# Kernel tuning notes

Hardware: AMD Instinct MI355X
Metric: run time of the kernel (lower is better)

## Reference

```python
import jax, jax.numpy as jnp
import numpy as np

B, S, DIM, H = 2, 2048, 1024, 16
HD = DIM // H  # head dim = 64


def setup_inputs() -> dict:
    key = jax.random.key(0)
    ks = jax.random.split(key, 10)
    scale = 1.0 / np.sqrt(DIM)
    x = jax.random.normal(ks[0], (B, S, DIM), dtype=jnp.float32)
    # per-head projection weights stacked over heads: [H, DIM, HD]
    Wq = jax.random.normal(ks[1], (H, DIM, HD), dtype=jnp.float32) * scale
    bq = jax.random.normal(ks[2], (H, HD), dtype=jnp.float32) * 0.01
    Wk = jax.random.normal(ks[3], (H, DIM, HD), dtype=jnp.float32) * scale
    bk = jax.random.normal(ks[4], (H, HD), dtype=jnp.float32) * 0.01
    Wv = jax.random.normal(ks[5], (H, DIM, HD), dtype=jnp.float32) * scale
    bv = jax.random.normal(ks[6], (H, HD), dtype=jnp.float32) * 0.01
    # output linear: [DIM, DIM]
    Wo = jax.random.normal(ks[7], (DIM, DIM), dtype=jnp.float32) * scale
    bo = jax.random.normal(ks[8], (DIM,), dtype=jnp.float32) * 0.01
    return {"x": x, "Wq": Wq, "bq": bq, "Wk": Wk, "bk": bk,
            "Wv": Wv, "bv": bv, "Wo": Wo, "bo": bo}


def reference(x, Wq, bq, Wk, bk, Wv, bv, Wo, bo):
    # per-head projections: [B, H, S, HD]
    q = jnp.einsum('bsd,hde->bhse', x, Wq) + bq[None, :, None, :]
    k = jnp.einsum('bsd,hde->bhse', x, Wk) + bk[None, :, None, :]
    v = jnp.einsum('bsd,hde->bhse', x, Wv) + bv[None, :, None, :]
    # causal attention scores: [B, H, S, S], scaled by sqrt(head_dim)
    scores = jnp.einsum('bhse,bhte->bhst', q, k) / jnp.sqrt(jnp.float32(HD))
    causal = jnp.tril(jnp.ones((S, S), dtype=bool))
    scores = jnp.where(causal[None, None], scores, -jnp.inf)
    attn = jax.nn.softmax(scores, axis=-1)
    out = jnp.einsum('bhst,bhte->bhse', attn, v)  # [B, H, S, HD]
    # concat heads in order -> [B, S, DIM]
    out = out.transpose(0, 2, 1, 3).reshape(B, S, DIM)
    return out @ Wo + bo
```

## Files before the change

### kernel.cpp

```cpp
#include <hip/hip_runtime.h>

typedef _Float16 half8 __attribute__((ext_vector_type(8)));
typedef _Float16 half4 __attribute__((ext_vector_type(4)));
typedef float f32x4 __attribute__((ext_vector_type(4)));

#define MFMA32(a, b, c) __builtin_amdgcn_mfma_f32_16x16x32_f16((a), (b), (c), 0, 0, 0)
#define MFMA16(a, b, c) __builtin_amdgcn_mfma_f32_16x16x16f16((a), (b), (c), 0, 0, 0)

static constexpr int Bc = 2, Sc = 2048, DIMc = 1024, Hc = 16, HDc = 64;
static constexpr int Mc = Bc * Sc;
static constexpr int NQKV = 3 * DIMc;

__device__ __forceinline__ void gl_lds16(const _Float16* g, _Float16* l) {
  __builtin_amdgcn_global_load_lds(
      (const __attribute__((address_space(1))) void*)g,
      (__attribute__((address_space(3))) void*)l, 16, 0, 0);
}


__global__ __launch_bounds__(256) void k_prep_all(
    const float* __restrict__ x, const float* __restrict__ Wq,
    const float* __restrict__ Wk, const float* __restrict__ Wv,
    const float* __restrict__ Wo, _Float16* __restrict__ xh,
    _Float16* __restrict__ WallT, _Float16* __restrict__ WoT) {
  __shared__ float Ls[64 * 65];
  const int bx = blockIdx.x, tid = threadIdx.x;
  if (bx < 2048) {
    const int i = bx * 256 + tid;
    const float4* xf = (const float4*)x;
    float4 a = xf[i * 2], b = xf[i * 2 + 1];
    half8 hv;
    hv[0] = (_Float16)a.x; hv[1] = (_Float16)a.y;
    hv[2] = (_Float16)a.z; hv[3] = (_Float16)a.w;
    hv[4] = (_Float16)b.x; hv[5] = (_Float16)b.y;
    hv[6] = (_Float16)b.z; hv[7] = (_Float16)b.w;
    *(half8*)&xh[(size_t)i * 8] = hv;
    return;
  }
  int b2 = bx - 2048;
  if (b2 < 768) {
    const int dt = b2 & 15, ph = b2 >> 4;
    const int p = ph >> 4, h = ph & 15;
    const float* W = (p == 0) ? Wq : (p == 1) ? Wk : Wv;
    for (int c = tid; c < 4096; c += 256) {
      int dr = c >> 6, e = c & 63;
      Ls[e * 65 + dr] = W[h * 65536 + (dt * 64 + dr) * 64 + e];
    }
    __syncthreads();
    for (int c = tid; c < 4096; c += 256) {
      int e = c >> 6, dr = c & 63;
      WallT[(size_t)(p * 1024 + h * 64 + e) * 1024 + dt * 64 + dr] = (_Float16)Ls[e * 65 + dr];
    }
  } else {
    int b3 = b2 - 768;
    const int dt = b3 & 15, nt = b3 >> 4;
    for (int c = tid; c < 4096; c += 256) {
      int dr = c >> 6, nl = c & 63;
      Ls[nl * 65 + dr] = Wo[(dt * 64 + dr) * 1024 + nt * 64 + nl];
    }
    __syncthreads();
    for (int c = tid; c < 4096; c += 256) {
      int nl = c >> 6, dr = c & 63;
      WoT[(size_t)(nt * 64 + nl) * 1024 + dt * 64 + dr] = (_Float16)Ls[nl * 65 + dr];
    }
  }
}


#define STAGE_AB(buf, kk0)                                                     \
    for (int it = 0; it < 2; ++it) {                                           \
      int idx = it * 256 + tid;                                                \
      int row = idx >> 2, scb = (idx & 3) ^ ((row >> 1) & 3);                  \
      gl_lds16(&A[(size_t)(m0 + row) * DIMc + (kk0) + scb * 8],                \
               &As[buf][(it * 256 + wave * 64) * 8]);                          \
    }                                                                          \
    for (int it = 0; it < 2; ++it) {                                           \
      int idx = it * 256 + tid;                                                \
      int row = idx >> 2, scb = (idx & 3) ^ ((row >> 1) & 3);                  \
      gl_lds16(&Bt[(size_t)(n0 + row) * DIMc + (kk0) + scb * 8],               \
               &Bs[buf][(it * 256 + wave * 64) * 8]);                          \
    }

#define GEMM_CORE_COOP()                                                       \
  __shared__ _Float16 As[2][128 * 32];                                         \
  __shared__ _Float16 Bs[2][128 * 32];                                         \
  const int tid = threadIdx.x;                                                 \
  const int lane = tid & 63, wave = tid >> 6;                                  \
  const int quad = lane >> 4, mr = lane & 15;                                  \
  const int sl = quad ^ ((mr >> 1) & 3);                                       \
  const int wm = wave >> 1, wn = wave & 1;                                     \
  f32x4 acc[4][4];                                                             \
  for (int i = 0; i < 4; i++)                                                  \
    for (int j = 0; j < 4; j++) acc[i][j] = f32x4{0.f, 0.f, 0.f, 0.f};         \
  STAGE_AB(0, 0)                                                               \
  for (int k0 = 0; k0 < DIMc; k0 += 32) {                                      \
    const int cur = (k0 >> 5) & 1;                                             \
    if (k0 + 32 < DIMc) {                                                      \
      STAGE_AB(cur ^ 1, k0 + 32)                                               \
      asm volatile("s_waitcnt vmcnt(4)" ::: "memory");                         \
    } else {                                                                   \
      asm volatile("s_waitcnt vmcnt(0)" ::: "memory");                         \
    }                                                                          \
    __builtin_amdgcn_s_barrier();                                              \
    __builtin_amdgcn_sched_barrier(0);                                         \
    half8 af[4], bf[4];                                                        \
    for (int i = 0; i < 4; i++)                                                \
      af[i] = *(const half8*)&As[cur][(wm * 64 + i * 16 + mr) * 32 + sl * 8];  \
    for (int i = 0; i < 4; i++)                                                \
      bf[i] = *(const half8*)&Bs[cur][(wn * 64 + i * 16 + mr) * 32 + sl * 8];  \
    for (int i = 0; i < 4; i++)                                                \
      for (int j = 0; j < 4; j++) acc[i][j] = MFMA32(af[i], bf[j], acc[i][j]); \
    asm volatile("s_waitcnt lgkmcnt(0)" ::: "memory");                         \
    __builtin_amdgcn_s_barrier();                                              \
    __builtin_amdgcn_sched_barrier(0);                                         \
  }


#define STAGE_WP(buf, kk0)                                                     \
  {                                                                            \
    const int r_ = lane >> 2;                                                  \
    const int c_ = ((lane & 3) ^ ((r_ >> 1) & 3)) * 8;                         \
    for (int it = 0; it < 4; ++it)                                             \
      gl_lds16(&Arow[(size_t)(it * 16 + r_) * DIMc + (kk0) + c_],              \
               &SH[wave][buf][0][it * 512]);                                   \
    for (int it = 0; it < 4; ++it)                                             \
      gl_lds16(&Brow[(size_t)(it * 16 + r_) * DIMc + (kk0) + c_],              \
               &SH[wave][buf][1][it * 512]);                                   \
  }

#define COMPUTE_WP(buf)                                                        \
  {                                                                            \
    half8 af[4], bf[4];                                                        \
    for (int i = 0; i < 4; i++)                                                \
      af[i] = *(const half8*)&SH[wave][buf][0][(i * 16 + mr) * 32 + sl];       \
    for (int i = 0; i < 4; i++)                                                \
      bf[i] = *(const half8*)&SH[wave][buf][1][(i * 16 + mr) * 32 + sl];       \
    for (int i = 0; i < 4; i++)                                                \
      for (int j = 0; j < 4; j++) acc[i][j] = MFMA32(af[i], bf[j], acc[i][j]); \
  }

#define GEMM_CORE_WP()                                                         \
  __shared__ _Float16 SH[4][2][2][64 * 32];        \
  const int tid = threadIdx.x;                                                 \
  const int lane = tid & 63, wave = tid >> 6;                                  \
  const int quad = lane >> 4, mr = lane & 15;                                  \
  const int sl = (quad ^ ((mr >> 1) & 3)) * 8;                                 \
  const int wm = wave >> 1, wn = wave & 1;                                     \
  const _Float16* Arow = A + (size_t)(m0 + wm * 64) * DIMc;                    \
  const _Float16* Brow = Bt + (size_t)(n0 + wn * 64) * DIMc;                   \
  f32x4 acc[4][4];                                                             \
  for (int i = 0; i < 4; i++)                                                  \
    for (int j = 0; j < 4; j++) acc[i][j] = f32x4{0.f, 0.f, 0.f, 0.f};         \
  STAGE_WP(0, 0)                                                               \
  for (int k0 = 0; k0 < DIMc; k0 += 64) {                                      \
    STAGE_WP(1, k0 + 32)                                                       \
    asm volatile("s_waitcnt vmcnt(8)" ::: "memory");                           \
    __builtin_amdgcn_sched_barrier(0);                                         \
    COMPUTE_WP(0)                                                              \
    __builtin_amdgcn_sched_barrier(0);                                         \
    if (k0 + 64 < DIMc) {                                                      \
      STAGE_WP(0, k0 + 64)                                                     \
      asm volatile("s_waitcnt vmcnt(8)" ::: "memory");                         \
    } else {                                                                   \
      asm volatile("s_waitcnt vmcnt(0)" ::: "memory");                         \
    }                                                                          \
    __builtin_amdgcn_sched_barrier(0);                                         \
    COMPUTE_WP(1)                                                              \
    __builtin_amdgcn_sched_barrier(0);                                         \
  }

__global__ __launch_bounds__(256, 3) void k_gemm_qkv(
    const _Float16* __restrict__ xh, const _Float16* __restrict__ WallT,
    const float* __restrict__ bq, const float* __restrict__ bk,
    const float* __restrict__ bv, _Float16* __restrict__ qh,
    _Float16* __restrict__ kh, _Float16* __restrict__ vT) {
  const int bid = blockIdx.x;
  const int id = (bid & 7) * 96 + (bid >> 3);
  const bool qkrole = id < 512;
  const _Float16* A;
  const _Float16* Bt;
  int m0, n0;
  if (qkrole) {
    A = xh; Bt = WallT;
    n0 = (id & 15) * 128; m0 = (id >> 4) * 128;
  } else {
    int j = id - 512;
    A = WallT + (size_t)2048 * DIMc; Bt = xh;
    n0 = (j & 31) * 128; m0 = (j >> 5) * 128;
  }
  GEMM_CORE_COOP()
  if (qkrole) {
    for (int i = 0; i < 4; i++) {
      for (int j = 0; j < 4; j++) {
        int col = n0 + wn * 64 + j * 16 + mr;
        int p = col >> 10, rem = col & 1023;
        const float* bias = p ? bk : bq;
        _Float16* dst = p ? kh : qh;
        float bb = bias[rem];
        int h = rem >> 6, e = rem & 63;
        for (int r = 0; r < 4; r++) {
          int row = m0 + wm * 64 + i * 16 + quad * 4 + r;
          int b = row >> 11, s = row & 2047;
          dst[(((size_t)(b * Hc + h)) * Sc + s) * HDc + e] = (_Float16)(acc[i][j][r] + bb);
        }
      }
    }
  } else {
    for (int i = 0; i < 4; i++) {
      int rowb = m0 + wm * 64 + i * 16 + quad * 4;
      for (int j = 0; j < 4; j++) {
        int col = n0 + wn * 64 + j * 16 + mr;
        int b = col >> 11, s = col & 2047;
        for (int r = 0; r < 4; r++) {
          int row = rowb + r;
          vT[(size_t)(b * 1024 + row) * Sc + s] = (_Float16)(acc[i][j][r] + bv[row]);
        }
      }
    }
  }
}

__global__ __launch_bounds__(256, 2) void k_gemm_out(
    const _Float16* __restrict__ A, const _Float16* __restrict__ Bt,
    const float* __restrict__ bo, float* __restrict__ out) {
  const int fid = blockIdx.y * 8 + blockIdx.x;
  const int id = (fid & 7) * 32 + (fid >> 3);
  const int m0 = (id >> 3) * 128, n0 = (id & 7) * 128;
  GEMM_CORE_WP()
  for (int i = 0; i < 4; i++) {
    for (int j = 0; j < 4; j++) {
      int col = n0 + wn * 64 + j * 16 + mr;
      float bb = bo[col];
      for (int r = 0; r < 4; r++) {
        int row = m0 + wm * 64 + i * 16 + quad * 4 + r;
        out[(size_t)row * DIMc + col] = acc[i][j][r] + bb;
      }
    }
  }
}


__global__ __launch_bounds__(256, 3) void k_attn(
    const _Float16* __restrict__ qg, const _Float16* __restrict__ kg,
    const _Float16* __restrict__ vTg, _Float16* __restrict__ att) {
  const int bid = blockIdx.x;
  const int qt = 31 - (bid >> 5);
  const int bh = bid & 31;
  const int b = bh >> 4, h = bh & 15;
  const int tid = threadIdx.x, w = tid >> 6, lane = tid & 63;
  const int quad = lane >> 4, mr = lane & 15, m7 = mr & 7, m3 = mr & 3;
  const size_t base = (size_t)bh * (Sc * HDc);
  const _Float16* Kg = kg + base;
  const _Float16* Vg = vTg + ((size_t)b * 1024 + h * 64) * Sc;

  __shared__ _Float16 Ks[4][2048];
  __shared__ _Float16 Vs[4][2][2048];
  __shared__ float Lsh[4][64];

  const int q0 = qt * 64;
  const int ntt = 2 * qt + 2;
  const int myn = (w < ntt) ? ((ntt - 1 - w) >> 2) + 1 : 0;

  const _Float16 qsc = (_Float16)(0.125f * 1.44269504f);
  half8 aq[4][2];
  for (int qf = 0; qf < 4; ++qf)
    for (int c = 0; c < 2; ++c) {
      half8 v = *(const half8*)&qg[base + (size_t)(q0 + qf * 16 + mr) * 64 + c * 32 + quad * 8];
      for (int j = 0; j < 8; ++j) v[j] = v[j] * qsc;
      aq[qf][c] = v;
    }

  f32x4 o[4][4];
  f32x4 ol[4];
  for (int nf = 0; nf < 4; ++nf)
    for (int qf = 0; qf < 4; ++qf) o[nf][qf] = f32x4{0.f, 0.f, 0.f, 0.f};
  for (int qf = 0; qf < 4; ++qf) ol[qf] = f32x4{0.f, 0.f, 0.f, 0.f};
  const half4 ones = {(_Float16)1.f, (_Float16)1.f, (_Float16)1.f, (_Float16)1.f};

#define STAGE_K(tt)                                                            \
  {                                                                            \
    const _Float16* ks = Kg + (size_t)(tt) * 2048;                             \
    for (int it = 0; it < 4; ++it) {                                           \
      int idx = it * 64 + lane;                                                \
      int row = idx >> 3, scb = (idx & 7) ^ (row & 7);                         \
      gl_lds16(ks + (size_t)row * 64 + scb * 8, &Ks[w][it * 512]);             \
    }                                                                          \
  }
#define STAGE_V(dst, tt)                                                       \
  {                                                                            \
    const _Float16* vs = Vg + (tt) * 32;                                       \
    for (int it = 0; it < 4; ++it) {                                           \
      int idx = it * 64 + lane;                                                \
      int row = idx >> 2, scb = (idx & 3) ^ (row & 3);                         \
      gl_lds16(vs + (size_t)row * Sc + scb * 8, (dst) + it * 512);             \
    }                                                                          \
  }

  if (myn > 0) { STAGE_K(w) STAGE_V(&Vs[w][0][0], w) }
  asm volatile("s_waitcnt vmcnt(0)" ::: "memory");

  for (int i = 0; i < myn; ++i) {
    const int t = w + 4 * i;
    const _Float16* Vc = &Vs[w][i & 1][0];
    if (i + 1 < myn) STAGE_V(&Vs[w][(i + 1) & 1][0], t + 4)

    half8 kA[2][2];
    for (int kf = 0; kf < 2; ++kf) {
      const int r0 = (kf * 16 + mr) * 64;
      kA[kf][0] = *(const half8*)&Ks[w][r0 + ((quad ^ m7) * 8)];
      kA[kf][1] = *(const half8*)&Ks[w][r0 + (((quad ^ 4) ^ m7) * 8)];
    }
    asm volatile("s_waitcnt lgkmcnt(0)" ::: "memory");
    __builtin_amdgcn_sched_barrier(0);
    if (i + 1 < myn) STAGE_K(t + 4)

    __builtin_amdgcn_s_setprio(1);
    const int dg = (t - 2 * qt) * 32;
    half4 pf[4][2];
    for (int kf = 0; kf < 2; ++kf) {
      for (int qf = 0; qf < 4; ++qf) {
        f32x4 z = {0.f, 0.f, 0.f, 0.f};
        z = MFMA32(kA[kf][0], aq[qf][0], z);
        z = MFMA32(kA[kf][1], aq[qf][1], z);
        half4 pp;
        const int kvr = dg + kf * 16 + quad * 4;
        for (int r = 0; r < 4; ++r) {
          float p = __builtin_amdgcn_exp2f(z[r]);
          if (kvr + r > qf * 16 + mr) p = 0.f;
          pp[r] = (_Float16)p;
        }
        pf[qf][kf] = pp;
      }
    }

    for (int nf = 0; nf < 4; ++nf) {
      const int rb = (nf * 16 + mr) * 32;
      for (int kc = 0; kc < 2; ++kc) {
        int ch = kc * 2 + (quad >> 1);
        half4 vv = *(const half4*)&Vc[rb + ((ch ^ m3) * 8) + (quad & 1) * 4];
        for (int qf = 0; qf < 4; ++qf)
          o[nf][qf] = MFMA16(vv, pf[qf][kc], o[nf][qf]);
      }
    }
    for (int kc = 0; kc < 2; ++kc)
      for (int qf = 0; qf < 4; ++qf) ol[qf] = MFMA16(ones, pf[qf][kc], ol[qf]);
    __builtin_amdgcn_s_setprio(0);

    asm volatile("s_waitcnt vmcnt(0)" ::: "memory");
  }

  if (quad == 0)
    for (int qf = 0; qf < 4; ++qf) Lsh[w][qf * 16 + mr] = ol[qf][0];
  __syncthreads();

  const int q = tid & 63, eg = tid >> 6;
  const float linv = 1.0f / (Lsh[0][q] + Lsh[1][q] + Lsh[2][q] + Lsh[3][q]);
  float* Osh = (float*)&Ks[0][0];
  const size_t orow = ((size_t)(b * Sc + q0 + q)) * DIMc + h * 64;
  for (int nf = 0; nf < 4; ++nf) {
    for (int qf = 0; qf < 4; ++qf)
      for (int r = 0; r < 4; ++r)
        Osh[(w * 16 + quad * 4 + r) * 64 + qf * 16 + mr] = o[nf][qf][r];
    __syncthreads();
    half4 ov;
    for (int r = 0; r < 4; ++r) {
      int e = eg * 4 + r;
      float s = Osh[e * 64 + q] + Osh[(16 + e) * 64 + q] +
                Osh[(32 + e) * 64 + q] + Osh[(48 + e) * 64 + q];
      ov[r] = (_Float16)(s * linv);
    }
    *(half4*)&att[orow + nf * 16 + eg * 4] = ov;
    __syncthreads();
  }
#undef STAGE_K
#undef STAGE_V
}


extern "C" void kernel_launch(void* const* d_in, const int* in_sizes, int n_in,
                              void* d_out, int out_size, void* d_ws, size_t ws_size,
                              hipStream_t stream) {
  const float* x  = (const float*)d_in[0];
  const float* Wq = (const float*)d_in[1];
  const float* bq = (const float*)d_in[2];
  const float* Wk = (const float*)d_in[3];
  const float* bk = (const float*)d_in[4];
  const float* Wv = (const float*)d_in[5];
  const float* bv = (const float*)d_in[6];
  const float* Wo = (const float*)d_in[7];
  const float* bo = (const float*)d_in[8];
  float* out = (float*)d_out;

  _Float16* p = (_Float16*)d_ws;
  _Float16* xh    = p; p += (size_t)Mc * DIMc;
  _Float16* WallT = p; p += (size_t)NQKV * DIMc;
  _Float16* WoT   = p; p += (size_t)DIMc * DIMc;
  _Float16* qh    = p; p += (size_t)Bc * Hc * Sc * HDc;
  _Float16* kh    = p; p += (size_t)Bc * Hc * Sc * HDc;
  _Float16* vT    = p; p += (size_t)Bc * Hc * Sc * HDc;
  _Float16* atth  = p;

  k_prep_all<<<2048 + 768 + 256, 256, 0, stream>>>(x, Wq, Wk, Wv, Wo, xh, WallT, WoT);
  k_gemm_qkv<<<768, 256, 0, stream>>>(xh, WallT, bq, bk, bv, qh, kh, vT);
  k_attn<<<1024, 256, 0, stream>>>(qh, kh, vT, atth);
  k_gemm_out<<<dim3(DIMc / 128, Mc / 128), 256, 0, stream>>>(atth, WoT, bo, out);
}
```

Baseline: 179.8 us.

## Split attention over query rows per wave with shared double-buffered KV tiles

The attention kernel previously gave each wave a slice of the KV tiles for all 64 queries, then reduced the partial outputs and row sums across waves through shared memory. Now each wave owns 16 query rows, and all four waves cooperatively stage shared 64-row K/V tiles into double-buffered LDS with block barriers. This removes the cross-wave LDS reduction and its syncs, cuts per-wave register use (occupancy hint raised to 4), and shrinks LDS. In exchange it adds two block barriers per KV tile, and the diagonal tile is still fully computed with masking.

After: 180.9 us. No clear change (+0.6%).

```diff
diff --git a/kernel.cpp b/kernel.cpp
--- a/kernel.cpp
+++ b/kernel.cpp
@@ -162,7 +162,7 @@
       STAGE_WP(0, k0 + 64)                                                     \
       asm volatile("s_waitcnt vmcnt(8)" ::: "memory");                         \
     } else {                                                                   \
-      asm volatile("s_waitcnt vmcnt(0)" ::: "memory");                         \
+      asm volatile("s_waitcnt vmcnt(0)" ::: "memory");                        \
     }                                                                          \
     __builtin_amdgcn_sched_barrier(0);                                         \
     COMPUTE_WP(1)                                                              \
@@ -240,7 +240,7 @@
 }
 
 
-__global__ __launch_bounds__(256, 3) void k_attn(
+__global__ __launch_bounds__(256, 4) void k_attn(
     const _Float16* __restrict__ qg, const _Float16* __restrict__ kg,
     const _Float16* __restrict__ vTg, _Float16* __restrict__ att) {
   const int bid = blockIdx.x;
@@ -248,132 +248,106 @@
   const int bh = bid & 31;
   const int b = bh >> 4, h = bh & 15;
   const int tid = threadIdx.x, w = tid >> 6, lane = tid & 63;
-  const int quad = lane >> 4, mr = lane & 15, m7 = mr & 7, m3 = mr & 3;
+  const int quad = lane >> 4, mr = lane & 15, m7 = mr & 7;
   const size_t base = (size_t)bh * (Sc * HDc);
   const _Float16* Kg = kg + base;
   const _Float16* Vg = vTg + ((size_t)b * 1024 + h * 64) * Sc;
 
-  __shared__ _Float16 Ks[4][2048];
-  __shared__ _Float16 Vs[4][2][2048];
-  __shared__ float Lsh[4][64];
+  __shared__ _Float16 Kt[2][64 * 64];
+  __shared__ _Float16 Vt[2][64 * 64];
 
   const int q0 = qt * 64;
-  const int ntt = 2 * qt + 2;
-  const int myn = (w < ntt) ? ((ntt - 1 - w) >> 2) + 1 : 0;
+  const int nt = qt + 1;
 
   const _Float16 qsc = (_Float16)(0.125f * 1.44269504f);
-  half8 aq[4][2];
-  for (int qf = 0; qf < 4; ++qf)
-    for (int c = 0; c < 2; ++c) {
-      half8 v = *(const half8*)&qg[base + (size_t)(q0 + qf * 16 + mr) * 64 + c * 32 + quad * 8];
-      for (int j = 0; j < 8; ++j) v[j] = v[j] * qsc;
-      aq[qf][c] = v;
-    }
-
-  f32x4 o[4][4];
-  f32x4 ol[4];
-  for (int nf = 0; nf < 4; ++nf)
-    for (int qf = 0; qf < 4; ++qf) o[nf][qf] = f32x4{0.f, 0.f, 0.f, 0.f};
-  for (int qf = 0; qf < 4; ++qf) ol[qf] = f32x4{0.f, 0.f, 0.f, 0.f};
+  half8 aq[2];
+  for (int c = 0; c < 2; ++c) {
+    half8 v = *(const half8*)&qg[base + (size_t)(q0 + w * 16 + mr) * 64 + c * 32 + quad * 8];
+    for (int j = 0; j < 8; ++j) v[j] = v[j] * qsc;
+    aq[c] = v;
+  }
+
+  f32x4 o[4];
+  f32x4 ol;
+  for (int nf = 0; nf < 4; ++nf) o[nf] = f32x4{0.f, 0.f, 0.f, 0.f};
+  ol = f32x4{0.f, 0.f, 0.f, 0.f};
   const half4 ones = {(_Float16)1.f, (_Float16)1.f, (_Float16)1.f, (_Float16)1.f};
 
-#define STAGE_K(tt)                                                            \
+#define STAGE64(buf, tt)                                                       \
   {                                                                            \
-    const _Float16* ks = Kg + (size_t)(tt) * 2048;                             \
-    for (int it = 0; it < 4; ++it) {                                           \
-      int idx = it * 64 + lane;                                                \
+    const _Float16* ks = Kg + (size_t)(tt) * 4096;                             \
+    const _Float16* vs = Vg + (tt) * 64;                                       \
+    for (int it = 0; it < 2; ++it) {                                           \
+      int idx = it * 256 + tid;                                                \
       int row = idx >> 3, scb = (idx & 7) ^ (row & 7);                         \
-      gl_lds16(ks + (size_t)row * 64 + scb * 8, &Ks[w][it * 512]);             \
-    }                                                                          \
-  }
-#define STAGE_V(dst, tt)                                                       \
-  {                                                                            \
-    const _Float16* vs = Vg + (tt) * 32;                                       \
-    for (int it = 0; it < 4; ++it) {                                           \
-      int idx = it * 64 + lane;                                                \
-      int row = idx >> 2, scb = (idx & 3) ^ (row & 3);                         \
-      gl_lds16(vs + (size_t)row * Sc + scb * 8, (dst) + it * 512);             \
-    }                                                                          \
-  }
-
-  if (myn > 0) { STAGE_K(w) STAGE_V(&Vs[w][0][0], w) }
-  asm volatile("s_waitcnt vmcnt(0)" ::: "memory");
-
-  for (int i = 0; i < myn; ++i) {
-    const int t = w + 4 * i;
-    const _Float16* Vc = &Vs[w][i & 1][0];
-    if (i + 1 < myn) STAGE_V(&Vs[w][(i + 1) & 1][0], t + 4)
-
-    half8 kA[2][2];
-    for (int kf = 0; kf < 2; ++kf) {
+      gl_lds16(ks + (size_t)row * 64 + scb * 8,                                \
+               &Kt[buf][(it * 256 + w * 64) * 8]);                             \
+    }                                                                          \
+    for (int it = 0; it < 2; ++it) {                                           \
+      int idx = it * 256 + tid;                                                \
+      int row = idx >> 3, scb = (idx & 7) ^ (row & 7);                         \
+      gl_lds16(vs + (size_t)row * Sc + scb * 8,                                \
+               &Vt[buf][(it * 256 + w * 64) * 8]);                             \
+    }                                                                          \
+  }
+
+  STAGE64(0, 0)
+  for (int t = 0; t < nt; ++t) {
+    const int cur = t & 1;
+    if (t + 1 < nt) {
+      STAGE64(cur ^ 1, t + 1)
+      asm volatile("s_waitcnt vmcnt(4)" ::: "memory");
+    } else {
+      asm volatile("s_waitcnt vmcnt(0)" ::: "memory");
+    }
+    __builtin_amdgcn_s_barrier();
+    __builtin_amdgcn_sched_barrier(0);
+
+    __builtin_amdgcn_s_setprio(1);
+    const int dg = (t - qt) * 64;
+    half4 pf[4];
+    for (int kf = 0; kf < 4; ++kf) {
       const int r0 = (kf * 16 + mr) * 64;
-      kA[kf][0] = *(const half8*)&Ks[w][r0 + ((quad ^ m7) * 8)];
-      kA[kf][1] = *(const half8*)&Ks[w][r0 + (((quad ^ 4) ^ m7) * 8)];
-    }
+      half8 k0 = *(const half8*)&Kt[cur][r0 + ((quad ^ m7) * 8)];
+      half8 k1 = *(const half8*)&Kt[cur][r0 + (((quad ^ 4) ^ m7) * 8)];
+      f32x4 z = {0.f, 0.f, 0.f, 0.f};
+      z = MFMA32(k0, aq[0], z);
+      z = MFMA32(k1, aq[1], z);
+      half4 pp;
+      const int kvr = dg + kf * 16 + quad * 4;
+      const int qi = w * 16 + mr;
+      for (int r = 0; r < 4; ++r) {
+        float p = __builtin_amdgcn_exp2f(z[r]);
+        if (kvr + r > qi) p = 0.f;
+        pp[r] = (_Float16)p;
+      }
+      pf[kf] = pp;
+    }
+
+    for (int nf = 0; nf < 4; ++nf) {
+      const int er = (nf * 16 + mr) * 64;
+      for (int kc = 0; kc < 4; ++kc) {
+        int kb = kc * 2 + (quad >> 1);
+        half4 vv = *(const half4*)&Vt[cur][er + ((kb ^ m7) * 8) + (quad & 1) * 4];
+        o[nf] = MFMA16(vv, pf[kc], o[nf]);
+      }
+    }
+    for (int kc = 0; kc < 4; ++kc) ol = MFMA16(ones, pf[kc], ol);
+    __builtin_amdgcn_s_setprio(0);
+
     asm volatile("s_waitcnt lgkmcnt(0)" ::: "memory");
+    __builtin_amdgcn_s_barrier();
     __builtin_amdgcn_sched_barrier(0);
-    if (i + 1 < myn) STAGE_K(t + 4)
-
-    __builtin_amdgcn_s_setprio(1);
-    const int dg = (t - 2 * qt) * 32;
-    half4 pf[4][2];
-    for (int kf = 0; kf < 2; ++kf) {
-      for (int qf = 0; qf < 4; ++qf) {
-        f32x4 z = {0.f, 0.f, 0.f, 0.f};
-        z = MFMA32(kA[kf][0], aq[qf][0], z);
-        z = MFMA32(kA[kf][1], aq[qf][1], z);
-        half4 pp;
-        const int kvr = dg + kf * 16 + quad * 4;
-        for (int r = 0; r < 4; ++r) {
-          float p = __builtin_amdgcn_exp2f(z[r]);
-          if (kvr + r > qf * 16 + mr) p = 0.f;
-          pp[r] = (_Float16)p;
-        }
-        pf[qf][kf] = pp;
-      }
-    }
-
-    for (int nf = 0; nf < 4; ++nf) {
-      const int rb = (nf * 16 + mr) * 32;
-      for (int kc = 0; kc < 2; ++kc) {
-        int ch = kc * 2 + (quad >> 1);
-        half4 vv = *(const half4*)&Vc[rb + ((ch ^ m3) * 8) + (quad & 1) * 4];
-        for (int qf = 0; qf < 4; ++qf)
-          o[nf][qf] = MFMA16(vv, pf[qf][kc], o[nf][qf]);
-      }
-    }
-    for (int kc = 0; kc < 2; ++kc)
-      for (int qf = 0; qf < 4; ++qf) ol[qf] = MFMA16(ones, pf[qf][kc], ol[qf]);
-    __builtin_amdgcn_s_setprio(0);
-
-    asm volatile("s_waitcnt vmcnt(0)" ::: "memory");
-  }
-
-  if (quad == 0)
-    for (int qf = 0; qf < 4; ++qf) Lsh[w][qf * 16 + mr] = ol[qf][0];
-  __syncthreads();
-
-  const int q = tid & 63, eg = tid >> 6;
-  const float linv = 1.0f / (Lsh[0][q] + Lsh[1][q] + Lsh[2][q] + Lsh[3][q]);
-  float* Osh = (float*)&Ks[0][0];
-  const size_t orow = ((size_t)(b * Sc + q0 + q)) * DIMc + h * 64;
+  }
+
+  const float linv = 1.0f / ol[0];
+  const size_t orow = ((size_t)(b * Sc + q0 + w * 16 + mr)) * DIMc + h * 64;
   for (int nf = 0; nf < 4; ++nf) {
-    for (int qf = 0; qf < 4; ++qf)
-      for (int r = 0; r < 4; ++r)
-        Osh[(w * 16 + quad * 4 + r) * 64 + qf * 16 + mr] = o[nf][qf][r];
-    __syncthreads();
     half4 ov;
-    for (int r = 0; r < 4; ++r) {
-      int e = eg * 4 + r;
-      float s = Osh[e * 64 + q] + Osh[(16 + e) * 64 + q] +
-                Osh[(32 + e) * 64 + q] + Osh[(48 + e) * 64 + q];
-      ov[r] = (_Float16)(s * linv);
-    }
-    *(half4*)&att[orow + nf * 16 + eg * 4] = ov;
-    __syncthreads();
-  }
-#undef STAGE_K
-#undef STAGE_V
+    for (int r = 0; r < 4; ++r) ov[r] = (_Float16)(o[nf][r] * linv);
+    *(half4*)&att[orow + nf * 16 + quad * 4] = ov;
+  }
+#undef STAGE64
 }
 
 
```
